# Kernel optimization log

Measured on AMD Instinct MI355X. Metric: run time of the kernel, lower is better.

The kernel has to match this reference:

```python
import jax, jax.numpy as jnp
import numpy as np

# Faithful math of CuteInferMLP forward. The original quantizes X (and the GELU
# output D) into a per-token fp8 representation PLUS residual shift/sum fp8
# correction terms, so that the grouped fp8 GEMM reconstructs the full-precision
# product X @ W^T to near-fp16 accuracy. The reference therefore computes the
# exact target math: E = gelu(X @ W0^T + b0) @ W1^T + b1, with fp16 activation
# precision mimicked by casting, returned reshaped to (B, L, H).

def setup_inputs() -> dict:
    key = jax.random.key(0)
    k1, k2, k3, k4, k5 = jax.random.split(key, 5)
    B, L, H, N = 2, 2048, 2048, 8192
    x = jax.random.normal(k1, (B, L, H), dtype=jnp.float32)
    W0 = jax.random.normal(k2, (N, H), dtype=jnp.float32) * (1.0 / np.sqrt(H))
    bias0 = jax.random.normal(k3, (N,), dtype=jnp.float32) * 0.02
    W1 = jax.random.normal(k4, (H, N), dtype=jnp.float32) * (1.0 / np.sqrt(N))
    bias1 = jax.random.normal(k5, (H,), dtype=jnp.float32) * 0.02
    return {"x": x, "W0": W0, "bias0": bias0, "W1": W1, "bias1": bias1}

def reference(x, W0, bias0, W1, bias1):
    B, L, H = x.shape
    X = x.reshape(-1, H).astype(jnp.float16)          # (M, H), original casts fp32->fp16
    # GEMM 0 (NT layout): D = X @ W0^T + bias0, fused exact GELU
    D = jnp.dot(X.astype(jnp.float32), W0.T) + bias0  # (M, N)
    D = jax.nn.gelu(D, approximate=False).astype(jnp.float16)
    # GEMM 1 (NT layout): E = D @ W1^T + bias1
    E = jnp.dot(D.astype(jnp.float32), W1.T) + bias1  # (M, H)
    return E.astype(jnp.float16).reshape(B, L, H)
```

## Files before the change

### kernel.cpp

```cpp
#include <hip/hip_runtime.h>
#include <hip/hip_fp16.h>

typedef _Float16 half8  __attribute__((ext_vector_type(8)));
typedef _Float16 half4v __attribute__((ext_vector_type(4)));
typedef float    float4v __attribute__((ext_vector_type(4)));

#define BM 256
#define BN 128
#define BK 64
#define THREADS 512
#define BUFH 24576
#define LDS_BYTES (3 * BUFH * 2)

#define BAR() __builtin_amdgcn_s_barrier()
#define LGKM0() do { asm volatile("s_waitcnt lgkmcnt(0)" ::: "memory"); \
                     __builtin_amdgcn_sched_barrier(0); } while (0)
#define VMC(n) do { asm volatile("s_waitcnt vmcnt(" #n ")" ::: "memory"); \
                    __builtin_amdgcn_sched_barrier(0); } while (0)

__device__ __forceinline__ float gelu_exact(float v) {
    return 0.5f * v * (1.0f + erff(v * 0.70710678118654752f));
}

__device__ __forceinline__ void stage_half(const _Float16* __restrict__ g, int lda,
                                           _Float16* ldsdst, int tid) {
    const int r  = tid >> 3;
    const int ch = ((tid & 7) << 3) ^ ((r & 7) << 3);
    const int wslot = (tid >> 6) << 9;
    #pragma unroll
    for (int c = 0; c < 2; ++c) {
        __builtin_amdgcn_global_load_lds(
            (const __attribute__((address_space(1))) void*)(g + (size_t)(c * 64 + r) * lda + ch),
            (__attribute__((address_space(3))) void*)(ldsdst + c * 4096 + wslot),
            16, 0, 0);
    }
}

__global__ __launch_bounds__(256)
void cast_f32_f16_kernel(const float* __restrict__ in, _Float16* __restrict__ out, int n4) {
    int i = blockIdx.x * blockDim.x + threadIdx.x;
    const int stride = gridDim.x * blockDim.x;
    for (; i < n4; i += stride) {
        const float4v v = reinterpret_cast<const float4v*>(in)[i];
        half4v h;
        h[0] = (_Float16)v[0]; h[1] = (_Float16)v[1];
        h[2] = (_Float16)v[2]; h[3] = (_Float16)v[3];
        reinterpret_cast<half4v*>(out)[i] = h;
    }
}

template<int EPI>
__global__ __launch_bounds__(THREADS, 2)
void gemm8p(const _Float16* __restrict__ A, const _Float16* __restrict__ B,
            const float* __restrict__ bias, void* __restrict__ Cout,
            int M, int Nd, int K, int Mtiles, int Ntiles)
{
    extern __shared__ __align__(16) char smem[];
    _Float16* lds = (_Float16*)smem;

    const int tid  = threadIdx.x;
    const int lane = tid & 63;
    const int wid  = tid >> 6;
    const int wm   = wid >> 2;
    const int wn   = wid & 3;

    const int nwg = Mtiles * Ntiles;
    const int bid = blockIdx.x;
    const int swz = (bid & 7) * (nwg >> 3) + (bid >> 3);
    const int tm = swz % Mtiles;
    const int tn = swz / Mtiles;
    const int brow = tm * BM;
    const int bcol = tn * BN;

    const int frow = lane & 15;
    const int fk   = (lane >> 4) * 8;
    const int rA   = (lane >> 4) * 4;

    half8 pa, pb;
    #pragma unroll
    for (int e = 0; e < 8; ++e) {
        pa[e] = (_Float16)((frow == fk + e) ? 1.0f : 0.0f);
        pb[e] = (_Float16)(float)((fk + e) + 100 * frow);
    }
    float4v pd = {0.f, 0.f, 0.f, 0.f};
    pd = __builtin_amdgcn_mfma_f32_16x16x32_f16(pa, pb, pd, 0, 0, 0);
    const bool m1_ok = (pd[0] == (float)(rA + 0 + 100 * frow)) &&
                       (pd[1] == (float)(rA + 1 + 100 * frow));
    const bool swap_cd = (__ballot(m1_ok) != ~0ull);

    const int lrow = frow << 7;
    const int xr   = (lane & 7) << 4;
    const int g16  = ((lane >> 4) & 3) << 4;
    const int c0   = g16 ^ xr;
    const int c1   = (64 + g16) ^ xr;

    const _Float16* Ag0 = A + (size_t)brow * K;
    const _Float16* Ag1 = A + (size_t)(brow + 128) * K;
    const _Float16* Bg  = B + (size_t)bcol * K;

    const int NT = K >> 6;

    stage_half(Bg,       K, lds + 0 * BUFH + 16384, tid);
    stage_half(Ag0,      K, lds + 0 * BUFH,         tid);
    stage_half(Ag1,      K, lds + 0 * BUFH + 8192,  tid);
    stage_half(Bg  + 64, K, lds + 1 * BUFH + 16384, tid);
    stage_half(Ag0 + 64, K, lds + 1 * BUFH,         tid);
    stage_half(Ag1 + 64, K, lds + 1 * BUFH + 8192,  tid);
    VMC(6);
    BAR();

    float4v acc[8][2];
    #pragma unroll
    for (int m = 0; m < 8; ++m) {
        acc[m][0] = (float4v){0.f, 0.f, 0.f, 0.f};
        acc[m][1] = (float4v){0.f, 0.f, 0.f, 0.f};
    }

    half8 afr[4][2], bfr[2][2];

    int b0 = 0, b1 = 1, b2 = 2;
    for (int t = 0; t < NT; ++t) {
        const char* Lc   = (const char*)(lds + b0 * BUFH);
        _Float16*   Ln   = lds + b2 * BUFH;
        const char* Ablk = Lc + wm * 16384;
        const char* Bblk = Lc + 32768 + (wn << 12);
        const bool pre = (t + 2 < NT);

        #pragma unroll
        for (int fm = 0; fm < 4; ++fm) {
            afr[fm][0] = *(const half8*)(Ablk + (fm << 11) + lrow + c0);
            afr[fm][1] = *(const half8*)(Ablk + (fm << 11) + lrow + c1);
        }
        #pragma unroll
        for (int fn = 0; fn < 2; ++fn) {
            bfr[fn][0] = *(const half8*)(Bblk + (fn << 11) + lrow + c0);
            bfr[fn][1] = *(const half8*)(Bblk + (fn << 11) + lrow + c1);
        }
        if (pre) {
            stage_half(Bg  + (size_t)(t + 2) * 64, K, Ln + 16384, tid);
            stage_half(Ag0 + (size_t)(t + 2) * 64, K, Ln,         tid);
        }
        BAR();
        LGKM0();
        __builtin_amdgcn_s_setprio(1);
        #pragma unroll
        for (int ks = 0; ks < 2; ++ks)
            #pragma unroll
            for (int fm = 0; fm < 4; ++fm)
                #pragma unroll
                for (int fn = 0; fn < 2; ++fn)
                    acc[fm][fn] = __builtin_amdgcn_mfma_f32_16x16x32_f16(
                        afr[fm][ks], bfr[fn][ks], acc[fm][fn], 0, 0, 0);
        __builtin_amdgcn_s_setprio(0);
        BAR();

        #pragma unroll
        for (int fm = 0; fm < 4; ++fm) {
            afr[fm][0] = *(const half8*)(Ablk + ((4 + fm) << 11) + lrow + c0);
            afr[fm][1] = *(const half8*)(Ablk + ((4 + fm) << 11) + lrow + c1);
        }
        if (pre) stage_half(Ag1 + (size_t)(t + 2) * 64, K, Ln + 8192, tid);
        if (pre) { VMC(4); } else { VMC(0); }
        BAR();
        LGKM0();
        __builtin_amdgcn_s_setprio(1);
        #pragma unroll
        for (int ks = 0; ks < 2; ++ks)
            #pragma unroll
            for (int fm = 0; fm < 4; ++fm)
                #pragma unroll
                for (int fn = 0; fn < 2; ++fn)
                    acc[4 + fm][fn] = __builtin_amdgcn_mfma_f32_16x16x32_f16(
                        afr[fm][ks], bfr[fn][ks], acc[4 + fm][fn], 0, 0, 0);
        __builtin_amdgcn_s_setprio(0);
        BAR();

        const int tb = b0; b0 = b1; b1 = b2; b2 = tb;
    }

    #pragma unroll
    for (int fm = 0; fm < 8; ++fm) {
        #pragma unroll
        for (int fn = 0; fn < 2; ++fn) {
            #pragma unroll
            for (int g = 0; g < 4; ++g) {
                const int fr = swap_cd ? frow : (rA + g);
                const int fc = swap_cd ? (rA + g) : frow;
                const int gr = brow + wm * 128 + fm * 16 + fr;
                const int gc = bcol + wn * 32 + fn * 16 + fc;
                const float v = acc[fm][fn][g] + bias[gc];
                if constexpr (EPI == 0) {
                    ((_Float16*)Cout)[(size_t)gr * Nd + gc] = (_Float16)gelu_exact(v);
                } else {
                    ((float*)Cout)[(size_t)gr * Nd + gc] = (float)(_Float16)v;
                }
            }
        }
    }
}

extern "C" void kernel_launch(void* const* d_in, const int* in_sizes, int n_in,
                              void* d_out, int out_size, void* d_ws, size_t ws_size,
                              hipStream_t stream) {
    const float* x  = (const float*)d_in[0];
    const float* W0 = (const float*)d_in[1];
    const float* b0 = (const float*)d_in[2];
    const float* W1 = (const float*)d_in[3];
    const float* b1 = (const float*)d_in[4];

    const int N = in_sizes[2];
    const int H = in_sizes[4];
    const int M = in_sizes[0] / H;

    const size_t szX  = (size_t)M * H;
    const size_t szW0 = (size_t)N * H;
    const size_t szW1 = (size_t)H * N;

    _Float16* Xh  = (_Float16*)d_ws;
    _Float16* W0h = Xh + szX;
    _Float16* W1h = W0h + szW0;
    _Float16* D   = W1h + szW1;

    cast_f32_f16_kernel<<<2048, 256, 0, stream>>>(x,  Xh,  (int)(szX  / 4));
    cast_f32_f16_kernel<<<2048, 256, 0, stream>>>(W0, W0h, (int)(szW0 / 4));
    cast_f32_f16_kernel<<<2048, 256, 0, stream>>>(W1, W1h, (int)(szW1 / 4));

    (void)hipFuncSetAttribute(reinterpret_cast<const void*>(gemm8p<0>),
                              hipFuncAttributeMaxDynamicSharedMemorySize, LDS_BYTES);
    (void)hipFuncSetAttribute(reinterpret_cast<const void*>(gemm8p<1>),
                              hipFuncAttributeMaxDynamicSharedMemorySize, LDS_BYTES);

    gemm8p<0><<<dim3((M / BM) * (N / BN)), dim3(THREADS), LDS_BYTES, stream>>>(
        Xh, W0h, b0, D, M, N, H, M / BM, N / BN);
    gemm8p<1><<<dim3((M / BM) * (H / BN)), dim3(THREADS), LDS_BYTES, stream>>>(
        D, W1h, b1, d_out, M, H, N, M / BM, H / BN);
}
```

Before: 517.6 us.

## Enlarge per-wave GEMM tiles and switch to double-buffered pipeline with fewer barriers

Templates the GEMM on wave layout and thread count so each wave computes a 128x64 sub-tile instead of 128x32. The first GEMM uses a 256x256 block with 512 threads, and the second uses 256x128 with 256 threads. The triple-buffered, split-phase loop with four barriers per k-step is replaced by a double-buffered loop with one barrier per k-step and partial lgkmcnt waits. The aim is to raise MFMA-to-LDS-load reuse and cut synchronization. In exchange, the accumulator grows to 128 floats per lane, which at the requested occupancy may cause register spills, and prefetch depth drops to one tile.

Result: faster. 482.9 us (-6.7%).

```diff
diff --git a/kernel.cpp b/kernel.cpp
--- a/kernel.cpp
+++ b/kernel.cpp
@@ -5,15 +5,8 @@
 typedef _Float16 half4v __attribute__((ext_vector_type(4)));
 typedef float    float4v __attribute__((ext_vector_type(4)));
 
-#define BM 256
-#define BN 128
-#define BK 64
-#define THREADS 512
-#define BUFH 24576
-#define LDS_BYTES (3 * BUFH * 2)
-
 #define BAR() __builtin_amdgcn_s_barrier()
-#define LGKM0() do { asm volatile("s_waitcnt lgkmcnt(0)" ::: "memory"); \
+#define LGKM(n) do { asm volatile("s_waitcnt lgkmcnt(" #n ")" ::: "memory"); \
                      __builtin_amdgcn_sched_barrier(0); } while (0)
 #define VMC(n) do { asm volatile("s_waitcnt vmcnt(" #n ")" ::: "memory"); \
                     __builtin_amdgcn_sched_barrier(0); } while (0)
@@ -22,16 +15,17 @@
     return 0.5f * v * (1.0f + erff(v * 0.70710678118654752f));
 }
 
-__device__ __forceinline__ void stage_half(const _Float16* __restrict__ g, int lda,
-                                           _Float16* ldsdst, int tid) {
-    const int r  = tid >> 3;
-    const int ch = ((tid & 7) << 3) ^ ((r & 7) << 3);
-    const int wslot = (tid >> 6) << 9;
-    #pragma unroll
-    for (int c = 0; c < 2; ++c) {
+template<int T>
+__device__ __forceinline__ void stage_half(const _Float16* __restrict__ g, int ldk,
+                                           _Float16* dstbase, int tid) {
+    constexpr int RP = T / 8;
+    #pragma unroll
+    for (int p = 0; p < 128 / RP; ++p) {
+        const int r  = p * RP + (tid >> 3);
+        const int ch = ((tid & 7) << 3) ^ ((r & 7) << 3);
         __builtin_amdgcn_global_load_lds(
-            (const __attribute__((address_space(1))) void*)(g + (size_t)(c * 64 + r) * lda + ch),
-            (__attribute__((address_space(3))) void*)(ldsdst + c * 4096 + wslot),
+            (const __attribute__((address_space(1))) void*)(g + (size_t)r * ldk + ch),
+            (__attribute__((address_space(3))) void*)(dstbase + p * RP * 64 + (tid >> 6) * 512),
             16, 0, 0);
     }
 }
@@ -49,28 +43,27 @@
     }
 }
 
-template<int EPI>
-__global__ __launch_bounds__(THREADS, 2)
-void gemm8p(const _Float16* __restrict__ A, const _Float16* __restrict__ B,
-            const float* __restrict__ bias, void* __restrict__ Cout,
-            int M, int Nd, int K, int Mtiles, int Ntiles)
+template<int WN, int THREADS, int EPI>
+__global__ __launch_bounds__(THREADS, THREADS / 256)
+void gemm_pw(const _Float16* __restrict__ A, const _Float16* __restrict__ B,
+             const float* __restrict__ bias, void* __restrict__ Cout,
+             int M, int Nd, int K, int Mtiles, int Ntiles)
 {
+    constexpr int BUFH = 16384 + WN * 4096;
     extern __shared__ __align__(16) char smem[];
     _Float16* lds = (_Float16*)smem;
 
     const int tid  = threadIdx.x;
     const int lane = tid & 63;
     const int wid  = tid >> 6;
-    const int wm   = wid >> 2;
-    const int wn   = wid & 3;
+    const int wm   = (WN == 4) ? (wid >> 2) : (wid >> 1);
+    const int wn   = wid & (WN - 1);
 
     const int nwg = Mtiles * Ntiles;
     const int bid = blockIdx.x;
     const int swz = (bid & 7) * (nwg >> 3) + (bid >> 3);
-    const int tm = swz % Mtiles;
-    const int tn = swz / Mtiles;
-    const int brow = tm * BM;
-    const int bcol = tn * BN;
+    const int brow = (swz % Mtiles) * 256;
+    const int bcol = (swz / Mtiles) * (WN * 64);
 
     const int frow = lane & 15;
     const int fk   = (lane >> 4) * 8;
@@ -94,100 +87,99 @@
     const int c0   = g16 ^ xr;
     const int c1   = (64 + g16) ^ xr;
 
-    const _Float16* Ag0 = A + (size_t)brow * K;
-    const _Float16* Ag1 = A + (size_t)(brow + 128) * K;
-    const _Float16* Bg  = B + (size_t)bcol * K;
+    const _Float16* Ag = A + (size_t)brow * K;
+    const _Float16* Bg = B + (size_t)bcol * K;
+
+    auto stage_tile = [&](int kt, int buf) {
+        _Float16* base = lds + buf * BUFH;
+        const _Float16* ga = Ag + (size_t)kt * 64;
+        stage_half<THREADS>(ga,                  K, base,         tid);
+        stage_half<THREADS>(ga + (size_t)128*K,  K, base + 8192,  tid);
+        const _Float16* gb = Bg + (size_t)kt * 64;
+        stage_half<THREADS>(gb,                  K, base + 16384, tid);
+        if constexpr (WN == 4)
+            stage_half<THREADS>(gb + (size_t)128*K, K, base + 24576, tid);
+    };
 
     const int NT = K >> 6;
 
-    stage_half(Bg,       K, lds + 0 * BUFH + 16384, tid);
-    stage_half(Ag0,      K, lds + 0 * BUFH,         tid);
-    stage_half(Ag1,      K, lds + 0 * BUFH + 8192,  tid);
-    stage_half(Bg  + 64, K, lds + 1 * BUFH + 16384, tid);
-    stage_half(Ag0 + 64, K, lds + 1 * BUFH,         tid);
-    stage_half(Ag1 + 64, K, lds + 1 * BUFH + 8192,  tid);
-    VMC(6);
+    stage_tile(0, 0);
+    VMC(0);
     BAR();
 
-    float4v acc[8][2];
-    #pragma unroll
-    for (int m = 0; m < 8; ++m) {
-        acc[m][0] = (float4v){0.f, 0.f, 0.f, 0.f};
-        acc[m][1] = (float4v){0.f, 0.f, 0.f, 0.f};
-    }
-
-    half8 afr[4][2], bfr[2][2];
-
-    int b0 = 0, b1 = 1, b2 = 2;
+    float4v acc[8][4];
+    #pragma unroll
+    for (int m = 0; m < 8; ++m)
+        #pragma unroll
+        for (int n = 0; n < 4; ++n)
+            acc[m][n] = (float4v){0.f, 0.f, 0.f, 0.f};
+
+    int cur = 0;
     for (int t = 0; t < NT; ++t) {
-        const char* Lc   = (const char*)(lds + b0 * BUFH);
-        _Float16*   Ln   = lds + b2 * BUFH;
-        const char* Ablk = Lc + wm * 16384;
-        const char* Bblk = Lc + 32768 + (wn << 12);
-        const bool pre = (t + 2 < NT);
-
-        #pragma unroll
-        for (int fm = 0; fm < 4; ++fm) {
-            afr[fm][0] = *(const half8*)(Ablk + (fm << 11) + lrow + c0);
-            afr[fm][1] = *(const half8*)(Ablk + (fm << 11) + lrow + c1);
+        const char* bufc = (const char*)(lds + cur * BUFH);
+        const char* Ablk = bufc + wm * 16384;
+        const char* Bblk = bufc + 32768 + wn * 8192;
+        const bool  pre  = (t + 1 < NT);
+
+        half8 a[8][2], b0[2][2], b1[2][2];
+        #pragma unroll
+        for (int fm = 0; fm < 8; ++fm) {
+            a[fm][0] = *(const half8*)(Ablk + fm * 2048 + lrow + c0);
+            a[fm][1] = *(const half8*)(Ablk + fm * 2048 + lrow + c1);
         }
         #pragma unroll
         for (int fn = 0; fn < 2; ++fn) {
-            bfr[fn][0] = *(const half8*)(Bblk + (fn << 11) + lrow + c0);
-            bfr[fn][1] = *(const half8*)(Bblk + (fn << 11) + lrow + c1);
-        }
-        if (pre) {
-            stage_half(Bg  + (size_t)(t + 2) * 64, K, Ln + 16384, tid);
-            stage_half(Ag0 + (size_t)(t + 2) * 64, K, Ln,         tid);
-        }
-        BAR();
-        LGKM0();
+            b0[fn][0] = *(const half8*)(Bblk + fn * 2048 + lrow + c0);
+            b0[fn][1] = *(const half8*)(Bblk + fn * 2048 + lrow + c1);
+        }
+        if (pre) stage_tile(t + 1, cur ^ 1);
+        #pragma unroll
+        for (int fn = 0; fn < 2; ++fn) {
+            b1[fn][0] = *(const half8*)(Bblk + (2 + fn) * 2048 + lrow + c0);
+            b1[fn][1] = *(const half8*)(Bblk + (2 + fn) * 2048 + lrow + c1);
+        }
+
+        LGKM(4);
         __builtin_amdgcn_s_setprio(1);
         #pragma unroll
         for (int ks = 0; ks < 2; ++ks)
             #pragma unroll
-            for (int fm = 0; fm < 4; ++fm)
+            for (int fm = 0; fm < 8; ++fm)
                 #pragma unroll
                 for (int fn = 0; fn < 2; ++fn)
                     acc[fm][fn] = __builtin_amdgcn_mfma_f32_16x16x32_f16(
-                        afr[fm][ks], bfr[fn][ks], acc[fm][fn], 0, 0, 0);
+                        a[fm][ks], b0[fn][ks], acc[fm][fn], 0, 0, 0);
         __builtin_amdgcn_s_setprio(0);
-        BAR();
-
-        #pragma unroll
-        for (int fm = 0; fm < 4; ++fm) {
-            afr[fm][0] = *(const half8*)(Ablk + ((4 + fm) << 11) + lrow + c0);
-            afr[fm][1] = *(const half8*)(Ablk + ((4 + fm) << 11) + lrow + c1);
-        }
-        if (pre) stage_half(Ag1 + (size_t)(t + 2) * 64, K, Ln + 8192, tid);
-        if (pre) { VMC(4); } else { VMC(0); }
-        BAR();
-        LGKM0();
+
+        LGKM(0);
         __builtin_amdgcn_s_setprio(1);
         #pragma unroll
         for (int ks = 0; ks < 2; ++ks)
             #pragma unroll
-            for (int fm = 0; fm < 4; ++fm)
+            for (int fm = 0; fm < 8; ++fm)
                 #pragma unroll
                 for (int fn = 0; fn < 2; ++fn)
-                    acc[4 + fm][fn] = __builtin_amdgcn_mfma_f32_16x16x32_f16(
-                        afr[fm][ks], bfr[fn][ks], acc[4 + fm][fn], 0, 0, 0);
+                    acc[fm][2 + fn] = __builtin_amdgcn_mfma_f32_16x16x32_f16(
+                        a[fm][ks], b1[fn][ks], acc[fm][2 + fn], 0, 0, 0);
         __builtin_amdgcn_s_setprio(0);
-        BAR();
-
-        const int tb = b0; b0 = b1; b1 = b2; b2 = tb;
+
+        if (pre) {
+            VMC(0);
+            BAR();
+            cur ^= 1;
+        }
     }
 
     #pragma unroll
     for (int fm = 0; fm < 8; ++fm) {
         #pragma unroll
-        for (int fn = 0; fn < 2; ++fn) {
+        for (int fn = 0; fn < 4; ++fn) {
             #pragma unroll
             for (int g = 0; g < 4; ++g) {
                 const int fr = swap_cd ? frow : (rA + g);
                 const int fc = swap_cd ? (rA + g) : frow;
                 const int gr = brow + wm * 128 + fm * 16 + fr;
-                const int gc = bcol + wn * 32 + fn * 16 + fc;
+                const int gc = bcol + wn * 64 + fn * 16 + fc;
                 const float v = acc[fm][fn][g] + bias[gc];
                 if constexpr (EPI == 0) {
                     ((_Float16*)Cout)[(size_t)gr * Nd + gc] = (_Float16)gelu_exact(v);
@@ -225,13 +217,15 @@
     cast_f32_f16_kernel<<<2048, 256, 0, stream>>>(W0, W0h, (int)(szW0 / 4));
     cast_f32_f16_kernel<<<2048, 256, 0, stream>>>(W1, W1h, (int)(szW1 / 4));
 
-    (void)hipFuncSetAttribute(reinterpret_cast<const void*>(gemm8p<0>),
-                              hipFuncAttributeMaxDynamicSharedMemorySize, LDS_BYTES);
-    (void)hipFuncSetAttribute(reinterpret_cast<const void*>(gemm8p<1>),
-                              hipFuncAttributeMaxDynamicSharedMemorySize, LDS_BYTES);
-
-    gemm8p<0><<<dim3((M / BM) * (N / BN)), dim3(THREADS), LDS_BYTES, stream>>>(
-        Xh, W0h, b0, D, M, N, H, M / BM, N / BN);
-    gemm8p<1><<<dim3((M / BM) * (H / BN)), dim3(THREADS), LDS_BYTES, stream>>>(
-        D, W1h, b1, d_out, M, H, N, M / BM, H / BN);
-}
+    const int lds0 = 2 * (16384 + 4 * 4096) * 2;
+    const int lds1 = 2 * (16384 + 2 * 4096) * 2;
+    (void)hipFuncSetAttribute(reinterpret_cast<const void*>(gemm_pw<4, 512, 0>),
+                              hipFuncAttributeMaxDynamicSharedMemorySize, lds0);
+    (void)hipFuncSetAttribute(reinterpret_cast<const void*>(gemm_pw<2, 256, 1>),
+                              hipFuncAttributeMaxDynamicSharedMemorySize, lds1);
+
+    gemm_pw<4, 512, 0><<<dim3((M / 256) * (N / 256)), dim3(512), lds0, stream>>>(
+        Xh, W0h, b0, D, M, N, H, M / 256, N / 256);
+    gemm_pw<2, 256, 1><<<dim3((M / 256) * (H / 128)), dim3(256), lds1, stream>>>(
+        D, W1h, b1, d_out, M, H, N, M / 256, H / 128);
+}
```
